# Kernel optimization log

Measured on AMD Instinct MI355X. Metric: run time of the kernel, lower is better.

## Reference

```python
import jax, jax.numpy as jnp
import numpy as np

B, S, D = 2, 2048, 1024
H, KS, VS = 16, 64, 64

def setup_inputs() -> dict:
    key = jax.random.key(0)
    ks = jax.random.split(key, 11)
    s = 1.0 / np.sqrt(D)
    return {
        "query": jax.random.normal(ks[0], (B, S, D), jnp.float32),
        "key":   jax.random.normal(ks[1], (B, S, D), jnp.float32),
        "value": jax.random.normal(ks[2], (B, S, D), jnp.float32),
        # weights stored [in, out] (transpose of torch Linear)
        "Wq": jax.random.normal(ks[3], (D, H * KS), jnp.float32) * s,
        "bq": jnp.zeros((H * KS,), jnp.float32),
        "Wk": jax.random.normal(ks[4], (D, H * KS), jnp.float32) * s,
        "bk": jnp.zeros((H * KS,), jnp.float32),
        "Wv": jax.random.normal(ks[5], (D, H * VS), jnp.float32) * s,
        "bv": jnp.zeros((H * VS,), jnp.float32),
        "Wo": jax.random.normal(ks[6], (H * VS, D), jnp.float32) * s,
        "bo": jnp.zeros((D,), jnp.float32),
    }

def reference(query, key, value, Wq, bq, Wk, bk, Wv, bv, Wo, bo):
    b = query.shape[0]
    # projections + split heads -> [B, H, S, d]
    Q = (query @ Wq + bq).reshape(b, -1, H, KS).transpose(0, 2, 1, 3)
    K = (key   @ Wk + bk).reshape(b, -1, H, KS).transpose(0, 2, 1, 3)
    V = (value @ Wv + bv).reshape(b, -1, H, VS).transpose(0, 2, 1, 3)
    scores = jnp.einsum('bhqd,bhkd->bhqk', Q, K) / jnp.sqrt(jnp.float32(KS))
    attn = jax.nn.softmax(scores, axis=-1)  # dropout_rate=0.0 -> identity
    ctx = jnp.einsum('bhqk,bhkd->bhqd', attn, V)  # [B,H,S,VS]
    ctx = ctx.transpose(0, 2, 1, 3).reshape(b, attn.shape[-1], H * VS)
    out = ctx @ Wo + bo
    return out, attn
```

## Files before the change

kernel.cpp:

```cpp
#include <hip/hip_runtime.h>
#include <stdint.h>


typedef _Float16 f16;
typedef f16 f16x4 __attribute__((ext_vector_type(4)));
typedef f16 f16x8 __attribute__((ext_vector_type(8)));
typedef float f32x4 __attribute__((ext_vector_type(4)));
typedef uint32_t u32;
typedef u32 u32x4 __attribute__((ext_vector_type(4)));

#define L2E 1.4426950408889634f

__device__ __forceinline__ void gload16(const void* g, void* l) {
    __builtin_amdgcn_global_load_lds((__attribute__((address_space(1))) void*)g,
                                     (__attribute__((address_space(3))) void*)l,
                                     16, 0, 0);
}

__global__ __launch_bounds__(256) void k_cvt(const float* __restrict__ q,
                                             const float* __restrict__ k,
                                             const float* __restrict__ v,
                                             f16* __restrict__ dst)
{
    int z = blockIdx.z;
    const float* s = (z == 0) ? q : (z == 1) ? k : v;
    size_t i = (size_t)blockIdx.x * 256 + threadIdx.x;
    float4 f = ((const float4*)s)[i];
    f16x4 o = {(f16)f.x, (f16)f.y, (f16)f.z, (f16)f.w};
    *(f16x4*)(dst + (size_t)z * 4194304 + i * 4) = o;
}

__global__ __launch_bounds__(256) void k_wtrans(const float* __restrict__ w0,
                                                const float* __restrict__ w1,
                                                const float* __restrict__ w2,
                                                const float* __restrict__ w3,
                                                f16* __restrict__ wt)
{
    __shared__ f16 t[64][72];
    int z = blockIdx.z;
    const float* W = (z == 0) ? w0 : (z == 1) ? w1 : (z == 2) ? w2 : w3;
    f16* outp = wt + (size_t)z * 1048576;
    int tx = blockIdx.x, ty = blockIdx.y, tid = threadIdx.x;
#pragma unroll
    for (int r4 = 0; r4 < 4; r4++) {
        int row = r4 * 16 + (tid >> 4);
        int col = (tid & 15) * 4;
        float4 f = *(const float4*)(W + (size_t)(ty * 64 + row) * 1024 + tx * 64 + col);
        t[col + 0][row] = (f16)f.x; t[col + 1][row] = (f16)f.y;
        t[col + 2][row] = (f16)f.z; t[col + 3][row] = (f16)f.w;
    }
    __syncthreads();
#pragma unroll
    for (int cc = 0; cc < 2; cc++) {
        int c = tid + cc * 256;
        int row = c >> 3, ch = c & 7;
        f16x8 vv;
#pragma unroll
        for (int j = 0; j < 8; j++) vv[j] = t[row][ch * 8 + j];
        *(f16x8*)(outp + (size_t)(tx * 64 + row) * 1024 + ty * 64 + ch * 8) = vv;
    }
}

__global__ __launch_bounds__(256) void k_gemm(const f16* __restrict__ Ab,
                                              const f16* __restrict__ Wtb,
                                              const float* __restrict__ b0,
                                              const float* __restrict__ b1,
                                              const float* __restrict__ b2,
                                              void* __restrict__ o0,
                                              void* __restrict__ o1,
                                              int proj)
{
    __shared__ __align__(16) char As[16384];
    __shared__ __align__(16) char Bs[16384];
    const int tid = threadIdx.x;
    const int wv = tid >> 6, ln = tid & 63, lg = ln >> 4, li = ln & 15;
    const int m0 = blockIdx.y * 128, n0 = blockIdx.x * 128;
    const int wm = (wv >> 1) * 64, wn = (wv & 1) * 64;

    const f16* A; const f16* Bt; const float* bias; int mode;
    if (proj) {
        int z = blockIdx.z;
        A = Ab + (size_t)z * 4194304;
        Bt = Wtb + (size_t)z * 1048576;
        bias = (z == 0) ? b0 : (z == 1) ? b1 : b2;
        mode = (z == 2) ? 1 : 0;
    } else { A = Ab; Bt = Wtb; bias = b0; mode = 2; }

    const char* gA[4]; const char* gB[4];
#pragma unroll
    for (int c = 0; c < 4; c++) {
        int r = (wv * 4 + c) * 8 + (ln >> 3);
        int j = (ln & 7) ^ (r & 7);
        gA[c] = (const char*)A  + (size_t)(m0 + r) * 2048 + j * 16;
        gB[c] = (const char*)Bt + (size_t)(n0 + r) * 2048 + j * 16;
    }

    f32x4 acc[4][4] = {};
    for (int kt = 0; kt < 16; kt++) {
        __syncthreads();
#pragma unroll
        for (int c = 0; c < 4; c++) {
            gload16(gA[c] + kt * 128, As + (wv * 4 + c) * 1024);
            gload16(gB[c] + kt * 128, Bs + (wv * 4 + c) * 1024);
        }
        __syncthreads();
#pragma unroll
        for (int kk = 0; kk < 2; kk++) {
            f16x8 af[4], bf[4];
#pragma unroll
            for (int mi = 0; mi < 4; mi++) {
                int row = wm + mi * 16 + li;
                af[mi] = *(const f16x8*)(As + row * 128 + (((kk * 4 + lg) ^ (row & 7)) * 16));
            }
#pragma unroll
            for (int ni = 0; ni < 4; ni++) {
                int row = wn + ni * 16 + li;
                bf[ni] = *(const f16x8*)(Bs + row * 128 + (((kk * 4 + lg) ^ (row & 7)) * 16));
            }
#pragma unroll
            for (int mi = 0; mi < 4; mi++)
#pragma unroll
                for (int ni = 0; ni < 4; ni++)
                    acc[mi][ni] = __builtin_amdgcn_mfma_f32_16x16x32_f16(af[mi], bf[ni], acc[mi][ni], 0, 0, 0);
        }
    }

    float bvs[4];
#pragma unroll
    for (int ni = 0; ni < 4; ni++) bvs[ni] = bias[n0 + wn + ni * 16 + li];

    if (mode == 2) {
        float* O = (float*)o0;
#pragma unroll
        for (int mi = 0; mi < 4; mi++)
#pragma unroll
            for (int ni = 0; ni < 4; ni++) {
                int n = n0 + wn + ni * 16 + li;
#pragma unroll
                for (int r = 0; r < 4; r++) {
                    int m = m0 + wm + mi * 16 + lg * 4 + r;
                    O[(size_t)m * 1024 + n] = acc[mi][ni][r] + bvs[ni];
                }
            }
    } else if (mode == 0) {
        f16* O = (f16*)o0 + (size_t)blockIdx.z * 4194304;
#pragma unroll
        for (int mi = 0; mi < 4; mi++)
#pragma unroll
            for (int ni = 0; ni < 4; ni++) {
                int n = n0 + wn + ni * 16 + li;
                int h = n >> 6, d = n & 63;
#pragma unroll
                for (int r = 0; r < 4; r++) {
                    int m = m0 + wm + mi * 16 + lg * 4 + r;
                    int b = m >> 11, s = m & 2047;
                    O[(((size_t)b * 16 + h) * 2048 + s) * 64 + d] = (f16)(acc[mi][ni][r] + bvs[ni]);
                }
            }
    } else {
        f16* O = (f16*)o1;
#pragma unroll
        for (int mi = 0; mi < 4; mi++)
#pragma unroll
            for (int ni = 0; ni < 4; ni++) {
                int n = n0 + wn + ni * 16 + li;
                int h = n >> 6, d = n & 63;
                int mb = m0 + wm + mi * 16 + lg * 4;
                int b = mb >> 11, s = mb & 2047;
                f16x4 pk;
#pragma unroll
                for (int r = 0; r < 4; r++) pk[r] = (f16)(acc[mi][ni][r] + bvs[ni]);
                *(f16x4*)(O + (((size_t)b * 16 + h) * 64 + d) * 2048 + s) = pk;
            }
    }
}

__global__ __launch_bounds__(256, 3) void k_attn(const f16* __restrict__ Qb,
                                                 const f16* __restrict__ Kb,
                                                 const f16* __restrict__ Vt,
                                                 float* __restrict__ attn,
                                                 f16* __restrict__ ctx)
{
    __shared__ __align__(16) char Ks[16384];
    __shared__ __align__(16) char Ps[4][2048];
    const int tid = threadIdx.x, wv = tid >> 6, ln = tid & 63, lg = ln >> 4, li = ln & 15;
    const int bid = blockIdx.x;
    const int kk = bid >> 3;
    const int bh = (bid & 7) * 4 + (kk >> 5);
    const int q0 = (kk & 31) * 64 + wv * 16;

    const char* KbB = (const char*)Kb + (size_t)bh * 262144;
    const char* VtB = (const char*)Vt + (size_t)bh * 262144;

    const f16* qrow = Qb + ((size_t)bh * 2048 + q0 + li) * 64 + lg * 8;
    f16x8 aq0 = *(const f16x8*)(qrow);
    f16x8 aq1 = *(const f16x8*)(qrow + 32);
#pragma unroll
    for (int j = 0; j < 8; j++) {
        aq0[j] = (f16)((float)aq0[j] * 0.125f);
        aq1[j] = (f16)((float)aq1[j] * 0.125f);
    }

    float lacc[4] = {0.f, 0.f, 0.f, 0.f};
    {
        int rr[4], swp[4];
        const char* gp[4];
#pragma unroll
        for (int t = 0; t < 4; t++) {
            int c = tid + t * 256;
            int r = c >> 3, j = c & 7;
            rr[t] = r;
            swp[t] = r * 128 + ((j ^ (r & 7)) * 16);
            gp[t] = KbB + (size_t)r * 128 + j * 16;
        }
        u32x4 s[4];
#pragma unroll
        for (int t = 0; t < 4; t++) s[t] = *(const u32x4*)(gp[t]);
        for (int kt = 0; kt < 16; kt++) {
            __syncthreads();
#pragma unroll
            for (int t = 0; t < 4; t++) *(u32x4*)(Ks + swp[t]) = s[t];
            __syncthreads();
            if (kt + 1 < 16) {
#pragma unroll
                for (int t = 0; t < 4; t++) s[t] = *(const u32x4*)(gp[t] + (size_t)(kt + 1) * 16384);
            }
#pragma unroll
            for (int cf = 0; cf < 8; cf++) {
                int row = cf * 16 + li;
                f16x8 ak0 = *(const f16x8*)(Ks + row * 128 + ((lg ^ (row & 7)) * 16));
                f16x8 ak1 = *(const f16x8*)(Ks + row * 128 + (((4 + lg) ^ (row & 7)) * 16));
                f32x4 z = {0.f, 0.f, 0.f, 0.f};
                z = __builtin_amdgcn_mfma_f32_16x16x32_f16(ak0, aq0, z, 0, 0, 0);
                z = __builtin_amdgcn_mfma_f32_16x16x32_f16(ak1, aq1, z, 0, 0, 0);
                lacc[cf & 3] += exp2f(z[0] * L2E) + exp2f(z[1] * L2E)
                              + exp2f(z[2] * L2E) + exp2f(z[3] * L2E);
            }
        }
    }
    float l_ = (lacc[0] + lacc[1]) + (lacc[2] + lacc[3]);
    l_ += __shfl_xor(l_, 16);
    l_ += __shfl_xor(l_, 32);
    const float inv_l = 1.0f / l_;
    float* aRow = attn + ((size_t)bh * 2048 + q0 + li) * 2048;
    char* Pw = Ps[wv];

    f32x4 cacc[4] = {};
    const int r0 = tid >> 3, j0 = tid & 7;
    const int r1 = (tid + 256) >> 3, j1 = (tid + 256) & 7;
    const int sw0 = r0 * 128 + ((j0 ^ (r0 & 7)) * 16);
    const int sw1 = r1 * 128 + ((j1 ^ (r1 & 7)) * 16);
    u32x4 sk0 = *(const u32x4*)(KbB + (size_t)r0 * 128 + j0 * 16);
    u32x4 sk1 = *(const u32x4*)(KbB + (size_t)r1 * 128 + j1 * 16);
    for (int kt = 0; kt < 32; kt++) {
        __syncthreads();
        *(u32x4*)(Ks + sw0) = sk0;
        *(u32x4*)(Ks + sw1) = sk1;
        __syncthreads();
        if (kt + 1 < 32) {
            sk0 = *(const u32x4*)(KbB + (size_t)((kt + 1) * 64 + r0) * 128 + j0 * 16);
            sk1 = *(const u32x4*)(KbB + (size_t)((kt + 1) * 64 + r1) * 128 + j1 * 16);
        }
        f16x8 vf[4][2];
#pragma unroll
        for (int df = 0; df < 4; df++) {
            const char* vr = VtB + (size_t)(df * 16 + li) * 4096 + kt * 128 + lg * 16;
            vf[df][0] = *(const f16x8*)vr;
            vf[df][1] = *(const f16x8*)(vr + 64);
        }
        f32x4 zz[4];
#pragma unroll
        for (int cf = 0; cf < 4; cf++) {
            int row = cf * 16 + li;
            f16x8 ak0 = *(const f16x8*)(Ks + row * 128 + ((lg ^ (row & 7)) * 16));
            f16x8 ak1 = *(const f16x8*)(Ks + row * 128 + (((4 + lg) ^ (row & 7)) * 16));
            f32x4 z = {0.f, 0.f, 0.f, 0.f};
            z = __builtin_amdgcn_mfma_f32_16x16x32_f16(ak0, aq0, z, 0, 0, 0);
            z = __builtin_amdgcn_mfma_f32_16x16x32_f16(ak1, aq1, z, 0, 0, 0);
            zz[cf] = z;
        }
#pragma unroll
        for (int cf = 0; cf < 4; cf++) {
            float p0 = exp2f(zz[cf][0] * L2E) * inv_l;
            float p1 = exp2f(zz[cf][1] * L2E) * inv_l;
            float p2 = exp2f(zz[cf][2] * L2E) * inv_l;
            float p3 = exp2f(zz[cf][3] * L2E) * inv_l;
            f32x4 fv = {p0, p1, p2, p3};
            __builtin_nontemporal_store(fv, (f32x4*)(aRow + kt * 64 + cf * 16 + lg * 4));
            f16x4 pk = {(f16)p0, (f16)p1, (f16)p2, (f16)p3};
            int c = cf * 2 + (lg >> 1);
            *(f16x4*)(Pw + li * 128 + ((c ^ (li & 7)) * 16) + (lg & 1) * 8) = pk;
        }
#pragma unroll
        for (int s2 = 0; s2 < 2; s2++) {
            f16x8 bp = *(const f16x8*)(Pw + li * 128 + (((s2 * 4 + lg) ^ (li & 7)) * 16));
#pragma unroll
            for (int df = 0; df < 4; df++)
                cacc[df] = __builtin_amdgcn_mfma_f32_16x16x32_f16(vf[df][s2], bp, cacc[df], 0, 0, 0);
        }
    }

    const int b = bh >> 4, h = bh & 15;
#pragma unroll
    for (int df = 0; df < 4; df++) {
        f16x4 pk;
#pragma unroll
        for (int r = 0; r < 4; r++) pk[r] = (f16)cacc[df][r];
        size_t mrow = (size_t)b * 2048 + q0 + li;
        size_t n = (size_t)h * 64 + df * 16 + lg * 4;
        *(f16x4*)(ctx + mrow * 1024 + n) = pk;
    }
}

extern "C" void kernel_launch(void* const* d_in, const int* in_sizes, int n_in,
                              void* d_out, int out_size, void* d_ws, size_t ws_size,
                              hipStream_t stream)
{
    const float* q  = (const float*)d_in[0];
    const float* k  = (const float*)d_in[1];
    const float* v  = (const float*)d_in[2];
    const float* Wq = (const float*)d_in[3];
    const float* bq = (const float*)d_in[4];
    const float* Wk = (const float*)d_in[5];
    const float* bk = (const float*)d_in[6];
    const float* Wv = (const float*)d_in[7];
    const float* bv = (const float*)d_in[8];
    const float* Wo = (const float*)d_in[9];
    const float* bo = (const float*)d_in[10];

    f16* W = (f16*)d_ws;
    float* out = (float*)d_out;
    float* attn = out + 4194304;

    f16* X   = W;
    f16* Wt  = W + 12582912;
    f16* QKb = W + 16777216;
    f16* Vt  = W + 25165824;
    f16* ctx = W + 29360128;

    k_cvt<<<dim3(4096, 1, 3), 256, 0, stream>>>(q, k, v, X);
    k_wtrans<<<dim3(16, 16, 4), 256, 0, stream>>>(Wq, Wk, Wv, Wo, Wt);
    k_gemm<<<dim3(8, 32, 3), 256, 0, stream>>>(X, Wt, bq, bk, bv, QKb, Vt, 1);
    k_attn<<<dim3(1024), 256, 0, stream>>>(QKb, QKb + 4194304, Vt, attn, ctx);
    k_gemm<<<dim3(8, 32, 1), 256, 0, stream>>>(ctx, Wt + 3145728, bo, bo, bo, out, nullptr, 0);
}
```

Before: 275.2 us.

## Double-buffer K tiles in LDS and raise wave priority around MFMAs

Both attention passes now use two LDS buffers for the K tile, so the next tile is written to the spare buffer while the current one is read. This removes one of the two barriers per iteration. s_setprio hints are also placed around the MFMA groups so the waves issuing matrix instructions get scheduling priority. The cost is double the K LDS footprint (32 KB plus P), which may lower occupancy below the requested three blocks per CU.

```diff
diff --git a/kernel.cpp b/kernel.cpp
--- a/kernel.cpp
+++ b/kernel.cpp
@@ -181,7 +181,7 @@
                                                  float* __restrict__ attn,
                                                  f16* __restrict__ ctx)
 {
-    __shared__ __align__(16) char Ks[16384];
+    __shared__ __align__(16) char Ks[32768];
     __shared__ __align__(16) char Ps[4][2048];
     const int tid = threadIdx.x, wv = tid >> 6, ln = tid & 63, lg = ln >> 4, li = ln & 15;
     const int bid = blockIdx.x;
@@ -203,39 +203,49 @@
 
     float lacc[4] = {0.f, 0.f, 0.f, 0.f};
     {
-        int rr[4], swp[4];
+        int swp[4];
         const char* gp[4];
 #pragma unroll
         for (int t = 0; t < 4; t++) {
             int c = tid + t * 256;
             int r = c >> 3, j = c & 7;
-            rr[t] = r;
             swp[t] = r * 128 + ((j ^ (r & 7)) * 16);
             gp[t] = KbB + (size_t)r * 128 + j * 16;
         }
         u32x4 s[4];
 #pragma unroll
         for (int t = 0; t < 4; t++) s[t] = *(const u32x4*)(gp[t]);
+#pragma unroll
+        for (int t = 0; t < 4; t++) *(u32x4*)(Ks + swp[t]) = s[t];
+#pragma unroll
+        for (int t = 0; t < 4; t++) s[t] = *(const u32x4*)(gp[t] + 16384);
+        __syncthreads();
         for (int kt = 0; kt < 16; kt++) {
-            __syncthreads();
-#pragma unroll
-            for (int t = 0; t < 4; t++) *(u32x4*)(Ks + swp[t]) = s[t];
-            __syncthreads();
+            const char* cur = Ks + (kt & 1) * 16384;
             if (kt + 1 < 16) {
-#pragma unroll
-                for (int t = 0; t < 4; t++) s[t] = *(const u32x4*)(gp[t] + (size_t)(kt + 1) * 16384);
+                char* nxt = Ks + ((kt + 1) & 1) * 16384;
+#pragma unroll
+                for (int t = 0; t < 4; t++) *(u32x4*)(nxt + swp[t]) = s[t];
+                if (kt + 2 < 16) {
+#pragma unroll
+                    for (int t = 0; t < 4; t++)
+                        s[t] = *(const u32x4*)(gp[t] + (size_t)(kt + 2) * 16384);
+                }
             }
 #pragma unroll
             for (int cf = 0; cf < 8; cf++) {
                 int row = cf * 16 + li;
-                f16x8 ak0 = *(const f16x8*)(Ks + row * 128 + ((lg ^ (row & 7)) * 16));
-                f16x8 ak1 = *(const f16x8*)(Ks + row * 128 + (((4 + lg) ^ (row & 7)) * 16));
+                f16x8 ak0 = *(const f16x8*)(cur + row * 128 + ((lg ^ (row & 7)) * 16));
+                f16x8 ak1 = *(const f16x8*)(cur + row * 128 + (((4 + lg) ^ (row & 7)) * 16));
+                __builtin_amdgcn_s_setprio(1);
                 f32x4 z = {0.f, 0.f, 0.f, 0.f};
                 z = __builtin_amdgcn_mfma_f32_16x16x32_f16(ak0, aq0, z, 0, 0, 0);
                 z = __builtin_amdgcn_mfma_f32_16x16x32_f16(ak1, aq1, z, 0, 0, 0);
+                __builtin_amdgcn_s_setprio(0);
                 lacc[cf & 3] += exp2f(z[0] * L2E) + exp2f(z[1] * L2E)
                               + exp2f(z[2] * L2E) + exp2f(z[3] * L2E);
             }
+            if (kt + 1 < 16) __syncthreads();
         }
     }
     float l_ = (lacc[0] + lacc[1]) + (lacc[2] + lacc[3]);
@@ -244,6 +254,8 @@
     const float inv_l = 1.0f / l_;
     float* aRow = attn + ((size_t)bh * 2048 + q0 + li) * 2048;
     char* Pw = Ps[wv];
+
+    __syncthreads();
 
     f32x4 cacc[4] = {};
     const int r0 = tid >> 3, j0 = tid & 7;
@@ -252,14 +264,21 @@
     const int sw1 = r1 * 128 + ((j1 ^ (r1 & 7)) * 16);
     u32x4 sk0 = *(const u32x4*)(KbB + (size_t)r0 * 128 + j0 * 16);
     u32x4 sk1 = *(const u32x4*)(KbB + (size_t)r1 * 128 + j1 * 16);
+    *(u32x4*)(Ks + sw0) = sk0;
+    *(u32x4*)(Ks + sw1) = sk1;
+    sk0 = *(const u32x4*)(KbB + (size_t)(64 + r0) * 128 + j0 * 16);
+    sk1 = *(const u32x4*)(KbB + (size_t)(64 + r1) * 128 + j1 * 16);
+    __syncthreads();
     for (int kt = 0; kt < 32; kt++) {
-        __syncthreads();
-        *(u32x4*)(Ks + sw0) = sk0;
-        *(u32x4*)(Ks + sw1) = sk1;
-        __syncthreads();
+        const char* cur = Ks + (kt & 1) * 8192;
         if (kt + 1 < 32) {
-            sk0 = *(const u32x4*)(KbB + (size_t)((kt + 1) * 64 + r0) * 128 + j0 * 16);
-            sk1 = *(const u32x4*)(KbB + (size_t)((kt + 1) * 64 + r1) * 128 + j1 * 16);
+            char* nxt = Ks + ((kt + 1) & 1) * 8192;
+            *(u32x4*)(nxt + sw0) = sk0;
+            *(u32x4*)(nxt + sw1) = sk1;
+            if (kt + 2 < 32) {
+                sk0 = *(const u32x4*)(KbB + (size_t)((kt + 2) * 64 + r0) * 128 + j0 * 16);
+                sk1 = *(const u32x4*)(KbB + (size_t)((kt + 2) * 64 + r1) * 128 + j1 * 16);
+            }
         }
         f16x8 vf[4][2];
 #pragma unroll
@@ -272,11 +291,13 @@
 #pragma unroll
         for (int cf = 0; cf < 4; cf++) {
             int row = cf * 16 + li;
-            f16x8 ak0 = *(const f16x8*)(Ks + row * 128 + ((lg ^ (row & 7)) * 16));
-            f16x8 ak1 = *(const f16x8*)(Ks + row * 128 + (((4 + lg) ^ (row & 7)) * 16));
+            f16x8 ak0 = *(const f16x8*)(cur + row * 128 + ((lg ^ (row & 7)) * 16));
+            f16x8 ak1 = *(const f16x8*)(cur + row * 128 + (((4 + lg) ^ (row & 7)) * 16));
+            __builtin_amdgcn_s_setprio(1);
             f32x4 z = {0.f, 0.f, 0.f, 0.f};
             z = __builtin_amdgcn_mfma_f32_16x16x32_f16(ak0, aq0, z, 0, 0, 0);
             z = __builtin_amdgcn_mfma_f32_16x16x32_f16(ak1, aq1, z, 0, 0, 0);
+            __builtin_amdgcn_s_setprio(0);
             zz[cf] = z;
         }
 #pragma unroll
@@ -294,10 +315,13 @@
 #pragma unroll
         for (int s2 = 0; s2 < 2; s2++) {
             f16x8 bp = *(const f16x8*)(Pw + li * 128 + (((s2 * 4 + lg) ^ (li & 7)) * 16));
+            __builtin_amdgcn_s_setprio(1);
 #pragma unroll
             for (int df = 0; df < 4; df++)
                 cacc[df] = __builtin_amdgcn_mfma_f32_16x16x32_f16(vf[df][s2], bp, cacc[df], 0, 0, 0);
-        }
+            __builtin_amdgcn_s_setprio(0);
+        }
+        if (kt + 1 < 32) __syncthreads();
     }
 
     const int b = bh >> 4, h = bh & 15;
```

Result: no change. 277.7 us (+0.9%).
